# Kernel optimization log

Hardware: AMD Instinct MI355X
Metric: run time of the kernel (lower is better)

## Reference

```python
import jax, jax.numpy as jnp
import numpy as np

RMIN, RMAX = -5.0, 5.0
MIN_BIN, MIN_SLOPE = 1e-4, 1e-4
BATCH, DIM, NBINS, HID = 65536, 64, 8, 128
NLAYERS = 6
SPLIT = DIM // 2  # 32
PDIM = 3 * NBINS + 1  # 25


def _mlp(h, w1, c1, w2, c2, w3, c3, w4, c4):
    # equinox MLP, depth=3: relu on hidden layers, identity on output
    h = jax.nn.relu(h @ w1.T + c1)
    h = jax.nn.relu(h @ w2.T + c2)
    h = jax.nn.relu(h @ w3.T + c3)
    return h @ w4.T + c4


def _rqs_forward(x, params):
    # x: [B,T], params: [B,T,3K+1] -> (y, logdet) each [B,T]
    K = (params.shape[-1] - 1) // 3
    total = RMAX - RMIN
    widths = jax.nn.softmax(params[..., :K], axis=-1) * (total - K * MIN_BIN) + MIN_BIN
    heights = jax.nn.softmax(params[..., K:2 * K], axis=-1) * (total - K * MIN_BIN) + MIN_BIN
    slope_off = float(np.log(np.exp(1.0 - MIN_SLOPE) - 1.0))
    slopes = jax.nn.softplus(params[..., 2 * K:] + slope_off) + MIN_SLOPE  # [B,T,K+1]
    zero = jnp.zeros(widths.shape[:-1] + (1,), widths.dtype)
    x_pos = jnp.concatenate([zero, jnp.cumsum(widths, -1)], -1) + RMIN   # [B,T,K+1]
    y_pos = jnp.concatenate([zero, jnp.cumsum(heights, -1)], -1) + RMIN
    below, above = x < RMIN, x > RMAX
    sl, sr = slopes[..., 0], slopes[..., -1]
    y_lin_l = (x - RMIN) * sl + RMIN
    y_lin_r = (x - RMAX) * sr + RMAX
    # searchsorted(x_pos[1:-1], x, side='right') == count of knots <= x
    bin_idx = jnp.clip(jnp.sum(x_pos[..., 1:-1] <= x[..., None], axis=-1), 0, K - 1)
    take = lambda a, i: jnp.take_along_axis(a, i[..., None], axis=-1)[..., 0]
    x_k, x_k1 = take(x_pos, bin_idx), take(x_pos, bin_idx + 1)
    y_k, y_k1 = take(y_pos, bin_idx), take(y_pos, bin_idx + 1)
    d_k, d_k1 = take(slopes, bin_idx), take(slopes, bin_idx + 1)
    w, h = x_k1 - x_k, y_k1 - y_k
    xi = jnp.clip((x - x_k) / w, 0.0, 1.0)
    s = h / w
    xi1m = 1.0 - xi
    q = xi * xi1m
    num = s * xi * xi + d_k * q
    den = s + (d_k1 + d_k - 2.0 * s) * q
    y_sp = y_k + h * num / den
    deriv = s * s * (d_k1 * xi * xi + 2.0 * s * q + d_k * xi1m * xi1m) / (den * den)
    y = jnp.where(below, y_lin_l, jnp.where(above, y_lin_r, y_sp))
    ld = jnp.where(below, jnp.log(sl), jnp.where(above, jnp.log(sr), jnp.log(deriv)))
    return y, ld


def _coupling(x, w1, c1, w2, c2, w3, c3, w4, c4, midx, tidx):
    xm = x[:, midx]           # [B,32]
    xt = x[:, tidx]           # [B,32]
    params = _mlp(xm, w1, c1, w2, c2, w3, c3, w4, c4)  # [B, 32*25]
    params = params.reshape(xt.shape[0], xt.shape[1], PDIM)
    yt, ld = _rqs_forward(xt, params)
    y = jnp.zeros_like(x).at[:, midx].set(xm).at[:, tidx].set(yt)
    return y, jnp.sum(ld, axis=-1)


def _make_masks():
    half_m = np.arange(0, SPLIT, dtype=np.int32)          # mask==1 positions
    half_t = np.arange(SPLIT, DIM, dtype=np.int32)
    alt_m = np.arange(1, DIM, 2, dtype=np.int32)          # odd -> mask==1
    alt_t = np.arange(0, DIM, 2, dtype=np.int32)
    mi = np.stack([half_m if i % 2 == 0 else alt_m for i in range(NLAYERS)])
    ti = np.stack([half_t if i % 2 == 0 else alt_t for i in range(NLAYERS)])
    return jnp.asarray(mi), jnp.asarray(ti)


def setup_inputs() -> dict:
    key = jax.random.key(0)
    ks = jax.random.split(key, 10)
    sc = 0.05
    x = jax.random.normal(ks[0], (BATCH, DIM), jnp.float32)
    W1 = jax.random.normal(ks[1], (NLAYERS, HID, SPLIT), jnp.float32) * sc
    b1 = jax.random.normal(ks[2], (NLAYERS, HID), jnp.float32) * sc
    W2 = jax.random.normal(ks[3], (NLAYERS, HID, HID), jnp.float32) * sc
    b2 = jax.random.normal(ks[4], (NLAYERS, HID), jnp.float32) * sc
    W3 = jax.random.normal(ks[5], (NLAYERS, HID, HID), jnp.float32) * sc
    b3 = jax.random.normal(ks[6], (NLAYERS, HID), jnp.float32) * sc
    W4 = jax.random.normal(ks[7], (NLAYERS, SPLIT * PDIM, HID), jnp.float32) * sc
    b4 = jax.random.normal(ks[8], (NLAYERS, SPLIT * PDIM), jnp.float32) * sc
    mask_idx, transform_idx = _make_masks()
    return dict(x=x, W1=W1, b1=b1, W2=W2, b2=b2, W3=W3, b3=b3, W4=W4, b4=b4,
                mask_idx=mask_idx, transform_idx=transform_idx)


def reference(x, W1, b1, W2, b2, W3, b3, W4, b4, mask_idx, transform_idx):
    def step(carry, layer):
        xc, tot = carry
        w1, c1, w2, c2, w3, c3, w4, c4, mi, ti = layer
        y, ld = _coupling(xc, w1, c1, w2, c2, w3, c3, w4, c4, mi, ti)
        return (y, tot + ld), None
    init = (x, jnp.zeros(x.shape[0], x.dtype))
    (y, total_logdet), _ = jax.lax.scan(
        step, init, (W1, b1, W2, b2, W3, b3, W4, b4, mask_idx, transform_idx))
    return y, total_logdet
```

## Files before the change

### kernel.cpp

```cpp
#include <hip/hip_runtime.h>
#include <math.h>

#define BATCH   65536
#define DIM     64
#define HID     128
#define SPLIT   32
#define NBINS   8
#define PDIM    25
#define NLAYERS 6
#define R_MIN   (-5.0f)
#define R_MAX   (5.0f)
#define MIN_BIN   1.0e-4f
#define MIN_SLOPE 1.0e-4f
#define SOFF      0.54116666f

#define ROWSW 16
#define WAVES 4
#define MBLK  64
#define NT    256

#define N_W1  (HID*SPLIT)
#define N_W2  (HID*HID)
#define N_W4P (32*32*HID)
#define N_W4  (SPLIT*PDIM*HID)

typedef __attribute__((ext_vector_type(8))) short bf16x8;
typedef __attribute__((ext_vector_type(4))) float f32x4;

__device__ __forceinline__ short f2bf(float f) {
    unsigned u = __builtin_bit_cast(unsigned, f);
    unsigned r = u + 0x7FFFu + ((u >> 16) & 1u);
    return (short)(r >> 16);
}

__device__ __forceinline__ unsigned pk2(float a, float b) {
    unsigned r;
    asm("v_cvt_pk_bf16_f32 %0, %1, %2" : "=v"(r) : "v"(a), "v"(b));
    return r;
}

__device__ __forceinline__ bf16x8 ldfrag(const short* base) {
    short4 lo = *reinterpret_cast<const short4*>(base);
    short4 hi = *reinterpret_cast<const short4*>(base + 64);
    bf16x8 a;
    a[0]=lo.x; a[1]=lo.y; a[2]=lo.z; a[3]=lo.w;
    a[4]=hi.x; a[5]=hi.y; a[6]=hi.z; a[7]=hi.w;
    return a;
}

__global__ void cvt_weights(const float* __restrict__ W1, const float* __restrict__ W2,
                            const float* __restrict__ W3, const float* __restrict__ W4,
                            const float* __restrict__ b4,
                            short* __restrict__ o1, short* __restrict__ o2,
                            short* __restrict__ o3, short* __restrict__ o4,
                            float* __restrict__ b4q) {
    const int stride = gridDim.x * blockDim.x;
    const int i0 = blockIdx.x * blockDim.x + threadIdx.x;
    for (int i = i0; i < NLAYERS*N_W1; i += stride) {
        const int L = i >> 12, rem = i & 4095;
        const int nt = rem >> 9, q = rem & 511;
        const int l = q >> 3, e = q & 7;
        o1[i] = f2bf(W1[L*N_W1 + (nt*16 + (l&15))*SPLIT + (l>>4)*8 + e]);
    }
    for (int i = i0; i < NLAYERS*N_W2; i += stride) {
        const int L = i >> 14, rem = i & 16383;
        const int c = rem >> 9, q = rem & 511;
        const int nt = c >> 2, kt = c & 3;
        const int l = q >> 3, e = q & 7;
        const int src = L*N_W2 + (nt*16 + (l&15))*HID + kt*32 + (l>>4)*8 + e;
        o2[i] = f2bf(W2[src]);
        o3[i] = f2bf(W3[src]);
    }
    for (int i = i0; i < NLAYERS*N_W4P; i += stride) {
        const int L = i >> 17, rem = i & (N_W4P - 1);
        const int c = rem >> 9, q = rem & 511;
        const int tb = c >> 5, pq = (c >> 2) & 7, kt = c & 3;
        const int l = q >> 3, e = q & 7;
        const int t = tb*4 + ((l & 15) >> 2);
        const int p = pq*4 + (l & 3);
        o4[i] = (p < PDIM)
              ? f2bf(W4[(size_t)L*N_W4 + (size_t)(t*PDIM + p)*HID + kt*32 + (l>>4)*8 + e])
              : (short)0;
    }
    for (int i = i0; i < NLAYERS*SPLIT*32; i += stride) {
        const int L = i >> 10, rem = i & 1023;
        const int t = rem >> 5, p = rem & 31;
        b4q[i] = (p < PDIM) ? b4[L*SPLIT*PDIM + t*PDIM + p] : 0.0f;
    }
}

__global__ __launch_bounds__(NT, 4) void flow_layer(
    const float* xin, float* yout, float* logdet, const int first,
    const short* __restrict__ bW1, const float* __restrict__ b1,
    const short* __restrict__ bW2, const float* __restrict__ b2,
    const short* __restrict__ bW3, const float* __restrict__ b3,
    const short* __restrict__ bW4, const float* __restrict__ b4q,
    const int* __restrict__ mi, const int* __restrict__ ti)
{
    __shared__ short act[WAVES][32 * 64];
    __shared__ float xts[WAVES][ROWSW][33];

    const int tid = threadIdx.x;
    const int wv  = tid >> 6;
    const int l   = tid & 63;
    const int lr  = l & 15;
    const int lg  = l >> 4;
    const int rbase = blockIdx.x * MBLK + wv * ROWSW;

    short* const actw = &act[wv][0];

    {
        const int kcol = l & 31;
        const int mc = mi[kcol], tc = ti[kcol];
        const int r0 = l >> 5;
        #pragma unroll
        for (int it = 0; it < 8; ++it) {
            const int r = r0 + it * 2;
            const float* row = xin + (size_t)(rbase + r) * DIM;
            const float mv = row[mc];
            actw[(kcol >> 2)*64 + r*4 + (kcol & 3)] = f2bf(mv);
            xts[wv][r][kcol] = row[tc];
            if (first) yout[(size_t)(rbase + r) * DIM + mc] = mv;
        }
    }

    {
        const bf16x8 afr = ldfrag(&actw[(2*lg)*64 + lr*4]);
        f32x4 c[8];
        #pragma unroll
        for (int nt = 0; nt < 8; ++nt) {
            const float4 bv = *reinterpret_cast<const float4*>(b1 + nt*16 + lg*4);
            c[nt] = (f32x4){bv.x, bv.y, bv.z, bv.w};
        }
        #pragma unroll
        for (int nt = 0; nt < 8; ++nt) {
            const bf16x8 wfr = *reinterpret_cast<const bf16x8*>(bW1 + (size_t)nt*512 + l*8);
            c[nt] = __builtin_amdgcn_mfma_f32_16x16x32_bf16(wfr, afr, c[nt], 0, 0, 0);
        }
        #pragma unroll
        for (int nt = 0; nt < 8; ++nt) {
            const unsigned u0 = pk2(fmaxf(c[nt][0], 0.0f), fmaxf(c[nt][1], 0.0f));
            const unsigned u1 = pk2(fmaxf(c[nt][2], 0.0f), fmaxf(c[nt][3], 0.0f));
            *reinterpret_cast<uint2*>(&actw[(nt*4 + lg)*64 + lr*4]) = (uint2){u0, u1};
        }
    }

    #pragma unroll 1
    for (int ph = 0; ph < 2; ++ph) {
        const short* Wp = ph ? bW3 : bW2;
        const float* bp = ph ? b3  : b2;
        bf16x8 afr[4];
        #pragma unroll
        for (int kt = 0; kt < 4; ++kt)
            afr[kt] = ldfrag(&actw[(kt*8 + 2*lg)*64 + lr*4]);
        f32x4 c[8];
        #pragma unroll
        for (int nt = 0; nt < 8; ++nt) {
            const float4 bv = *reinterpret_cast<const float4*>(bp + nt*16 + lg*4);
            c[nt] = (f32x4){bv.x, bv.y, bv.z, bv.w};
        }
        #pragma unroll
        for (int kt = 0; kt < 4; ++kt)
            #pragma unroll
            for (int nt = 0; nt < 8; ++nt) {
                const bf16x8 wfr = *reinterpret_cast<const bf16x8*>(Wp + (size_t)(nt*4 + kt)*512 + l*8);
                c[nt] = __builtin_amdgcn_mfma_f32_16x16x32_bf16(wfr, afr[kt], c[nt], 0, 0, 0);
            }
        #pragma unroll
        for (int nt = 0; nt < 8; ++nt) {
            const unsigned u0 = pk2(fmaxf(c[nt][0], 0.0f), fmaxf(c[nt][1], 0.0f));
            const unsigned u1 = pk2(fmaxf(c[nt][2], 0.0f), fmaxf(c[nt][3], 0.0f));
            *reinterpret_cast<uint2*>(&actw[(nt*4 + lg)*64 + lr*4]) = (uint2){u0, u1};
        }
    }

    bf16x8 afr[4];
    #pragma unroll
    for (int kt = 0; kt < 4; ++kt)
        afr[kt] = ldfrag(&actw[(kt*8 + 2*lg)*64 + lr*4]);

    float ldacc = 0.0f;
    #pragma unroll 1
    for (int tb = 0; tb < 8; ++tb) {
        const int t = tb*4 + lg;
        f32x4 c[8];
        #pragma unroll
        for (int pq = 0; pq < 8; ++pq) {
            const float4 bv = *reinterpret_cast<const float4*>(b4q + t*32 + pq*4);
            c[pq] = (f32x4){bv.x, bv.y, bv.z, bv.w};
        }
        #pragma unroll
        for (int kt = 0; kt < 4; ++kt)
            #pragma unroll
            for (int pq = 0; pq < 8; ++pq) {
                const bf16x8 wfr = *reinterpret_cast<const bf16x8*>(
                    bW4 + (size_t)((tb*8 + pq)*4 + kt)*512 + l*8);
                c[pq] = __builtin_amdgcn_mfma_f32_16x16x32_bf16(wfr, afr[kt], c[pq], 0, 0, 0);
            }

        float p[32];
        #pragma unroll
        for (int pq = 0; pq < 8; ++pq)
            #pragma unroll
            for (int j = 0; j < 4; ++j) p[pq*4 + j] = c[pq][j];

        float sl[NBINS + 1];
        #pragma unroll
        for (int i = 0; i < NBINS + 1; ++i) {
            const float z = p[2*NBINS + i] + SOFF;
            const float sp = (z > 15.0f) ? z : __logf(1.0f + __expf(z));
            sl[i] = sp + MIN_SLOPE;
        }
        float wd[NBINS];
        {
            float mx = p[0];
            #pragma unroll
            for (int i = 1; i < NBINS; ++i) mx = fmaxf(mx, p[i]);
            float sum = 0.0f;
            #pragma unroll
            for (int i = 0; i < NBINS; ++i) { wd[i] = __expf(p[i] - mx); sum += wd[i]; }
            const float sc = __fdividef((R_MAX - R_MIN) - NBINS * MIN_BIN, sum);
            #pragma unroll
            for (int i = 0; i < NBINS; ++i) wd[i] = wd[i] * sc + MIN_BIN;
        }
        float hg[NBINS];
        {
            float mx = p[NBINS];
            #pragma unroll
            for (int i = 1; i < NBINS; ++i) mx = fmaxf(mx, p[NBINS + i]);
            float sum = 0.0f;
            #pragma unroll
            for (int i = 0; i < NBINS; ++i) { hg[i] = __expf(p[NBINS + i] - mx); sum += hg[i]; }
            const float sc = __fdividef((R_MAX - R_MIN) - NBINS * MIN_BIN, sum);
            #pragma unroll
            for (int i = 0; i < NBINS; ++i) hg[i] = hg[i] * sc + MIN_BIN;
        }

        const float x = xts[wv][lr][t];

        int b = 0;
        {
            float cx = R_MIN;
            #pragma unroll
            for (int i = 1; i < NBINS; ++i) { cx += wd[i-1]; b += (cx <= x) ? 1 : 0; }
        }
        float x_k = R_MIN, y_k = R_MIN, wsel = wd[0], hsel = hg[0], d_k = sl[0], d_k1 = sl[1];
        {
            float cx = R_MIN, cy = R_MIN;
            #pragma unroll
            for (int i = 0; i < NBINS; ++i) {
                if (i == b) { x_k = cx; y_k = cy; wsel = wd[i]; hsel = hg[i];
                              d_k = sl[i]; d_k1 = sl[i+1]; }
                cx += wd[i]; cy += hg[i];
            }
        }

        const float invw = __fdividef(1.0f, wsel);
        float xi = (x - x_k) * invw;
        xi = fminf(fmaxf(xi, 0.0f), 1.0f);
        const float s    = hsel * invw;
        const float xi1m = 1.0f - xi;
        const float q    = xi * xi1m;
        const float num  = s * xi * xi + d_k * q;
        const float den  = s + (d_k1 + d_k - 2.0f * s) * q;
        const float invden = __fdividef(1.0f, den);
        const float y_sp = y_k + hsel * num * invden;
        const float deriv = s * s * (d_k1 * xi * xi + 2.0f * s * q + d_k * xi1m * xi1m)
                            * invden * invden;

        const bool below = x < R_MIN;
        const bool above = x > R_MAX;
        const float yv = below ? ((x - R_MIN) * sl[0]     + R_MIN)
                       : (above ? ((x - R_MAX) * sl[NBINS] + R_MAX) : y_sp);
        const float dv = below ? sl[0] : (above ? sl[NBINS] : deriv);
        ldacc += __logf(dv);

        yout[(size_t)(rbase + lr) * DIM + ti[t]] = yv;
    }

    ldacc += __shfl_xor(ldacc, 16, 64);
    ldacc += __shfl_xor(ldacc, 32, 64);
    if (l < 16) {
        const int row = rbase + lr;
        if (first) logdet[row] = ldacc;
        else       logdet[row] += ldacc;
    }
}

extern "C" void kernel_launch(void* const* d_in, const int* in_sizes, int n_in,
                              void* d_out, int out_size, void* d_ws, size_t ws_size,
                              hipStream_t stream) {
    const float* x  = (const float*)d_in[0];
    const float* W1 = (const float*)d_in[1];
    const float* b1 = (const float*)d_in[2];
    const float* W2 = (const float*)d_in[3];
    const float* b2 = (const float*)d_in[4];
    const float* W3 = (const float*)d_in[5];
    const float* b3 = (const float*)d_in[6];
    const float* W4 = (const float*)d_in[7];
    const float* b4 = (const float*)d_in[8];
    const int*   mi = (const int*)d_in[9];
    const int*   ti = (const int*)d_in[10];

    float* y      = (float*)d_out;
    float* logdet = y + (size_t)BATCH * DIM;

    short* bW1 = (short*)d_ws;
    short* bW2 = bW1 + NLAYERS * N_W1;
    short* bW3 = bW2 + NLAYERS * N_W2;
    short* bW4 = bW3 + NLAYERS * N_W2;
    float* b4q = (float*)(bW4 + (size_t)NLAYERS * N_W4P);

    cvt_weights<<<512, 256, 0, stream>>>(W1, W2, W3, W4, b4, bW1, bW2, bW3, bW4, b4q);

    dim3 grid(BATCH / MBLK), block(NT);
    for (int L = 0; L < NLAYERS; ++L) {
        flow_layer<<<grid, block, 0, stream>>>(
            (L == 0) ? x : y, y, logdet, (L == 0) ? 1 : 0,
            bW1 + (size_t)L * N_W1, b1 + L * HID,
            bW2 + (size_t)L * N_W2, b2 + L * HID,
            bW3 + (size_t)L * N_W2, b3 + L * HID,
            bW4 + (size_t)L * N_W4P, b4q + (size_t)L * SPLIT * 32,
            mi + L * SPLIT, ti + L * SPLIT);
    }
}
```

Baseline: 362.6 us.

## Stage MLP weights in LDS via async DMA with double-buffered W4 prefetch

Weights for all four MLP layers are copied into a shared LDS buffer with global_load_lds, so each block fetches them once instead of every wave reading them from global memory. The W4 tiles are double-buffered: the next output tile is prefetched while the current one is computed, and the matching transform-column x values are prefetched into registers. The all-zero padded parameter quad is no longer computed, cutting output MFMAs from 8 to 7 per tile. In exchange the kernel uses about 80KB of LDS, lowers launch bounds to 2 blocks per CU, and adds block-wide barriers each tile.

```diff
diff --git a/kernel.cpp b/kernel.cpp
--- a/kernel.cpp
+++ b/kernel.cpp
@@ -18,6 +18,7 @@
 #define WAVES 4
 #define MBLK  64
 #define NT    256
+#define W4CH  28
 
 #define N_W1  (HID*SPLIT)
 #define N_W2  (HID*HID)
@@ -37,6 +38,12 @@
     unsigned r;
     asm("v_cvt_pk_bf16_f32 %0, %1, %2" : "=v"(r) : "v"(a), "v"(b));
     return r;
+}
+
+__device__ __forceinline__ void gload16(const short* g, short* s) {
+    __builtin_amdgcn_global_load_lds(
+        (const __attribute__((address_space(1))) void*)g,
+        (__attribute__((address_space(3))) void*)s, 16, 0, 0);
 }
 
 __device__ __forceinline__ bf16x8 ldfrag(const short* base) {
@@ -89,7 +96,7 @@
     }
 }
 
-__global__ __launch_bounds__(NT, 4) void flow_layer(
+__global__ __launch_bounds__(NT, 2) void flow_layer(
     const float* xin, float* yout, float* logdet, const int first,
     const short* __restrict__ bW1, const float* __restrict__ b1,
     const short* __restrict__ bW2, const float* __restrict__ b2,
@@ -97,8 +104,8 @@
     const short* __restrict__ bW4, const float* __restrict__ b4q,
     const int* __restrict__ mi, const int* __restrict__ ti)
 {
+    __shared__ short wbuf[2][16384];
     __shared__ short act[WAVES][32 * 64];
-    __shared__ float xts[WAVES][ROWSW][33];
 
     const int tid = threadIdx.x;
     const int wv  = tid >> 6;
@@ -109,20 +116,30 @@
 
     short* const actw = &act[wv][0];
 
+    #pragma unroll
+    for (int i = 0; i < 2; ++i) {
+        const int c = wv * 2 + i;
+        gload16(bW1 + c * 512 + l * 8, &wbuf[0][c * 512]);
+    }
+    #pragma unroll
+    for (int i = 0; i < 8; ++i) {
+        const int c = wv * 8 + i;
+        gload16(bW2 + c * 512 + l * 8, &wbuf[1][c * 512]);
+    }
+
     {
         const int kcol = l & 31;
-        const int mc = mi[kcol], tc = ti[kcol];
+        const int mc = mi[kcol];
         const int r0 = l >> 5;
         #pragma unroll
         for (int it = 0; it < 8; ++it) {
             const int r = r0 + it * 2;
-            const float* row = xin + (size_t)(rbase + r) * DIM;
-            const float mv = row[mc];
+            const float mv = xin[(size_t)(rbase + r) * DIM + mc];
             actw[(kcol >> 2)*64 + r*4 + (kcol & 3)] = f2bf(mv);
-            xts[wv][r][kcol] = row[tc];
             if (first) yout[(size_t)(rbase + r) * DIM + mc] = mv;
         }
     }
+    __syncthreads();
 
     {
         const bf16x8 afr = ldfrag(&actw[(2*lg)*64 + lr*4]);
@@ -134,7 +151,7 @@
         }
         #pragma unroll
         for (int nt = 0; nt < 8; ++nt) {
-            const bf16x8 wfr = *reinterpret_cast<const bf16x8*>(bW1 + (size_t)nt*512 + l*8);
+            const bf16x8 wfr = *reinterpret_cast<const bf16x8*>(&wbuf[0][nt*512 + l*8]);
             c[nt] = __builtin_amdgcn_mfma_f32_16x16x32_bf16(wfr, afr, c[nt], 0, 0, 0);
         }
         #pragma unroll
@@ -144,11 +161,15 @@
             *reinterpret_cast<uint2*>(&actw[(nt*4 + lg)*64 + lr*4]) = (uint2){u0, u1};
         }
     }
-
-    #pragma unroll 1
-    for (int ph = 0; ph < 2; ++ph) {
-        const short* Wp = ph ? bW3 : bW2;
-        const float* bp = ph ? b3  : b2;
+    __syncthreads();
+
+    #pragma unroll
+    for (int i = 0; i < 8; ++i) {
+        const int c = wv * 8 + i;
+        gload16(bW3 + c * 512 + l * 8, &wbuf[0][c * 512]);
+    }
+
+    {
         bf16x8 afr[4];
         #pragma unroll
         for (int kt = 0; kt < 4; ++kt)
@@ -156,14 +177,47 @@
         f32x4 c[8];
         #pragma unroll
         for (int nt = 0; nt < 8; ++nt) {
-            const float4 bv = *reinterpret_cast<const float4*>(bp + nt*16 + lg*4);
+            const float4 bv = *reinterpret_cast<const float4*>(b2 + nt*16 + lg*4);
             c[nt] = (f32x4){bv.x, bv.y, bv.z, bv.w};
         }
         #pragma unroll
         for (int kt = 0; kt < 4; ++kt)
             #pragma unroll
             for (int nt = 0; nt < 8; ++nt) {
-                const bf16x8 wfr = *reinterpret_cast<const bf16x8*>(Wp + (size_t)(nt*4 + kt)*512 + l*8);
+                const bf16x8 wfr = *reinterpret_cast<const bf16x8*>(&wbuf[1][(nt*4 + kt)*512 + l*8]);
+                c[nt] = __builtin_amdgcn_mfma_f32_16x16x32_bf16(wfr, afr[kt], c[nt], 0, 0, 0);
+            }
+        #pragma unroll
+        for (int nt = 0; nt < 8; ++nt) {
+            const unsigned u0 = pk2(fmaxf(c[nt][0], 0.0f), fmaxf(c[nt][1], 0.0f));
+            const unsigned u1 = pk2(fmaxf(c[nt][2], 0.0f), fmaxf(c[nt][3], 0.0f));
+            *reinterpret_cast<uint2*>(&actw[(nt*4 + lg)*64 + lr*4]) = (uint2){u0, u1};
+        }
+    }
+    __syncthreads();
+
+    #pragma unroll
+    for (int i = 0; i < 7; ++i) {
+        const int c = wv * 7 + i;
+        gload16(bW4 + (size_t)c * 512 + l * 8, &wbuf[1][c * 512]);
+    }
+
+    {
+        bf16x8 afr[4];
+        #pragma unroll
+        for (int kt = 0; kt < 4; ++kt)
+            afr[kt] = ldfrag(&actw[(kt*8 + 2*lg)*64 + lr*4]);
+        f32x4 c[8];
+        #pragma unroll
+        for (int nt = 0; nt < 8; ++nt) {
+            const float4 bv = *reinterpret_cast<const float4*>(b3 + nt*16 + lg*4);
+            c[nt] = (f32x4){bv.x, bv.y, bv.z, bv.w};
+        }
+        #pragma unroll
+        for (int kt = 0; kt < 4; ++kt)
+            #pragma unroll
+            for (int nt = 0; nt < 8; ++nt) {
+                const bf16x8 wfr = *reinterpret_cast<const bf16x8*>(&wbuf[0][(nt*4 + kt)*512 + l*8]);
                 c[nt] = __builtin_amdgcn_mfma_f32_16x16x32_bf16(wfr, afr[kt], c[nt], 0, 0, 0);
             }
         #pragma unroll
@@ -179,28 +233,47 @@
     for (int kt = 0; kt < 4; ++kt)
         afr[kt] = ldfrag(&actw[(kt*8 + 2*lg)*64 + lr*4]);
 
+    __syncthreads();
+
+    const float* rowx = xin + (size_t)(rbase + lr) * DIM;
+    int   tcur = ti[lg];
+    float xcur = rowx[tcur];
+
     float ldacc = 0.0f;
     #pragma unroll 1
     for (int tb = 0; tb < 8; ++tb) {
+        if (tb < 7) {
+            short* wbn = &wbuf[tb & 1][0];
+            #pragma unroll
+            for (int i = 0; i < 7; ++i) {
+                const int c = wv * 7 + i;
+                gload16(bW4 + (size_t)((tb + 1) * 32 + c) * 512 + l * 8, wbn + c * 512);
+            }
+        }
+        int   tnxt = tcur;
+        float xnxt = xcur;
+        if (tb < 7) { tnxt = ti[(tb + 1) * 4 + lg]; xnxt = rowx[tnxt]; }
+
         const int t = tb*4 + lg;
-        f32x4 c[8];
-        #pragma unroll
-        for (int pq = 0; pq < 8; ++pq) {
+        const short* wb = &wbuf[(tb + 1) & 1][0];
+
+        f32x4 c[7];
+        #pragma unroll
+        for (int pq = 0; pq < 7; ++pq) {
             const float4 bv = *reinterpret_cast<const float4*>(b4q + t*32 + pq*4);
             c[pq] = (f32x4){bv.x, bv.y, bv.z, bv.w};
         }
         #pragma unroll
         for (int kt = 0; kt < 4; ++kt)
             #pragma unroll
-            for (int pq = 0; pq < 8; ++pq) {
-                const bf16x8 wfr = *reinterpret_cast<const bf16x8*>(
-                    bW4 + (size_t)((tb*8 + pq)*4 + kt)*512 + l*8);
+            for (int pq = 0; pq < 7; ++pq) {
+                const bf16x8 wfr = *reinterpret_cast<const bf16x8*>(wb + (pq*4 + kt)*512 + l*8);
                 c[pq] = __builtin_amdgcn_mfma_f32_16x16x32_bf16(wfr, afr[kt], c[pq], 0, 0, 0);
             }
 
-        float p[32];
-        #pragma unroll
-        for (int pq = 0; pq < 8; ++pq)
+        float p[28];
+        #pragma unroll
+        for (int pq = 0; pq < 7; ++pq)
             #pragma unroll
             for (int j = 0; j < 4; ++j) p[pq*4 + j] = c[pq][j];
 
@@ -236,7 +309,7 @@
             for (int i = 0; i < NBINS; ++i) hg[i] = hg[i] * sc + MIN_BIN;
         }
 
-        const float x = xts[wv][lr][t];
+        const float x = xcur;
 
         int b = 0;
         {
@@ -275,7 +348,10 @@
         const float dv = below ? sl[0] : (above ? sl[NBINS] : deriv);
         ldacc += __logf(dv);
 
-        yout[(size_t)(rbase + lr) * DIM + ti[t]] = yv;
+        yout[(size_t)(rbase + lr) * DIM + tcur] = yv;
+
+        __syncthreads();
+        tcur = tnxt; xcur = xnxt;
     }
 
     ldacc += __shfl_xor(ldacc, 16, 64);
```

New measurement: 351.7 us. 3.0% less time.

## Trim padded MFMA tile and compute softplus only for selected spline knots

Applied to the files above, without the earlier changes.

The last-layer GEMM now runs 7 column tiles instead of 8, skipping the tile that holds only padding beyond PDIM. The spline epilogue drops max-subtraction from both softmaxes, fuses the bin search with knot selection using selects, and evaluates softplus only for the two chosen slopes and the two boundary slopes instead of all nine. The per-row loop is templated with an optional unroll-by-2, and a different variant is chosen per layer. The aim is fewer MFMAs and transcendental ops in the epilogue. Removing max-subtraction gives up overflow protection for large logits, and the per-layer variant choice looks tuned to one measurement.

```diff
diff --git a/kernel.cpp b/kernel.cpp
--- a/kernel.cpp
+++ b/kernel.cpp
@@ -89,6 +89,7 @@
     }
 }
 
+template<int UNR>
 __global__ __launch_bounds__(NT, 4) void flow_layer(
     const float* xin, float* yout, float* logdet, const int first,
     const short* __restrict__ bW1, const float* __restrict__ b1,
@@ -180,80 +181,60 @@
         afr[kt] = ldfrag(&actw[(kt*8 + 2*lg)*64 + lr*4]);
 
     float ldacc = 0.0f;
-    #pragma unroll 1
-    for (int tb = 0; tb < 8; ++tb) {
+
+    auto body = [&](const int tb) {
         const int t = tb*4 + lg;
-        f32x4 c[8];
-        #pragma unroll
-        for (int pq = 0; pq < 8; ++pq) {
+        f32x4 c[7];
+        #pragma unroll
+        for (int pq = 0; pq < 7; ++pq) {
             const float4 bv = *reinterpret_cast<const float4*>(b4q + t*32 + pq*4);
             c[pq] = (f32x4){bv.x, bv.y, bv.z, bv.w};
         }
         #pragma unroll
         for (int kt = 0; kt < 4; ++kt)
             #pragma unroll
-            for (int pq = 0; pq < 8; ++pq) {
+            for (int pq = 0; pq < 7; ++pq) {
                 const bf16x8 wfr = *reinterpret_cast<const bf16x8*>(
                     bW4 + (size_t)((tb*8 + pq)*4 + kt)*512 + l*8);
                 c[pq] = __builtin_amdgcn_mfma_f32_16x16x32_bf16(wfr, afr[kt], c[pq], 0, 0, 0);
             }
 
-        float p[32];
-        #pragma unroll
-        for (int pq = 0; pq < 8; ++pq)
-            #pragma unroll
-            for (int j = 0; j < 4; ++j) p[pq*4 + j] = c[pq][j];
-
-        float sl[NBINS + 1];
-        #pragma unroll
-        for (int i = 0; i < NBINS + 1; ++i) {
-            const float z = p[2*NBINS + i] + SOFF;
-            const float sp = (z > 15.0f) ? z : __logf(1.0f + __expf(z));
-            sl[i] = sp + MIN_SLOPE;
-        }
-        float wd[NBINS];
-        {
-            float mx = p[0];
-            #pragma unroll
-            for (int i = 1; i < NBINS; ++i) mx = fmaxf(mx, p[i]);
-            float sum = 0.0f;
-            #pragma unroll
-            for (int i = 0; i < NBINS; ++i) { wd[i] = __expf(p[i] - mx); sum += wd[i]; }
-            const float sc = __fdividef((R_MAX - R_MIN) - NBINS * MIN_BIN, sum);
-            #pragma unroll
-            for (int i = 0; i < NBINS; ++i) wd[i] = wd[i] * sc + MIN_BIN;
-        }
-        float hg[NBINS];
-        {
-            float mx = p[NBINS];
-            #pragma unroll
-            for (int i = 1; i < NBINS; ++i) mx = fmaxf(mx, p[NBINS + i]);
-            float sum = 0.0f;
-            #pragma unroll
-            for (int i = 0; i < NBINS; ++i) { hg[i] = __expf(p[NBINS + i] - mx); sum += hg[i]; }
-            const float sc = __fdividef((R_MAX - R_MIN) - NBINS * MIN_BIN, sum);
-            #pragma unroll
-            for (int i = 0; i < NBINS; ++i) hg[i] = hg[i] * sc + MIN_BIN;
-        }
+#define P(i) c[(i)>>2][(i)&3]
+        float wd[NBINS], hg[NBINS];
+        float sw = 0.0f, sh = 0.0f;
+        #pragma unroll
+        for (int i = 0; i < NBINS; ++i) { wd[i] = __expf(P(i));         sw += wd[i]; }
+        #pragma unroll
+        for (int i = 0; i < NBINS; ++i) { hg[i] = __expf(P(NBINS + i)); sh += hg[i]; }
+        const float scw = __fdividef((R_MAX - R_MIN) - NBINS * MIN_BIN, sw);
+        const float sch = __fdividef((R_MAX - R_MIN) - NBINS * MIN_BIN, sh);
+        #pragma unroll
+        for (int i = 0; i < NBINS; ++i) { wd[i] = wd[i]*scw + MIN_BIN; hg[i] = hg[i]*sch + MIN_BIN; }
 
         const float x = xts[wv][lr][t];
 
-        int b = 0;
-        {
-            float cx = R_MIN;
-            #pragma unroll
-            for (int i = 1; i < NBINS; ++i) { cx += wd[i-1]; b += (cx <= x) ? 1 : 0; }
-        }
-        float x_k = R_MIN, y_k = R_MIN, wsel = wd[0], hsel = hg[0], d_k = sl[0], d_k1 = sl[1];
-        {
-            float cx = R_MIN, cy = R_MIN;
-            #pragma unroll
-            for (int i = 0; i < NBINS; ++i) {
-                if (i == b) { x_k = cx; y_k = cy; wsel = wd[i]; hsel = hg[i];
-                              d_k = sl[i]; d_k1 = sl[i+1]; }
-                cx += wd[i]; cy += hg[i];
-            }
-        }
+        float cx = R_MIN, cy = R_MIN;
+        float x_k = R_MIN, y_k = R_MIN, wsel = wd[0], hsel = hg[0];
+        float z0 = P(16), z1 = P(17);
+        #pragma unroll
+        for (int i = 1; i < NBINS; ++i) {
+            cx += wd[i-1]; cy += hg[i-1];
+            const bool tk = (cx <= x);
+            x_k  = tk ? cx        : x_k;
+            y_k  = tk ? cy        : y_k;
+            wsel = tk ? wd[i]     : wsel;
+            hsel = tk ? hg[i]     : hsel;
+            z0   = tk ? P(16 + i) : z0;
+            z1   = tk ? P(17 + i) : z1;
+        }
+
+        auto sp = [](float v) {
+            const float z = v + SOFF;
+            return ((z > 15.0f) ? z : __logf(1.0f + __expf(z))) + MIN_SLOPE;
+        };
+        const float d_k = sp(z0), d_k1 = sp(z1);
+        const float sl0 = sp(P(16)), sl8 = sp(P(24));
+#undef P
 
         const float invw = __fdividef(1.0f, wsel);
         float xi = (x - x_k) * invw;
@@ -270,12 +251,20 @@
 
         const bool below = x < R_MIN;
         const bool above = x > R_MAX;
-        const float yv = below ? ((x - R_MIN) * sl[0]     + R_MIN)
-                       : (above ? ((x - R_MAX) * sl[NBINS] + R_MAX) : y_sp);
-        const float dv = below ? sl[0] : (above ? sl[NBINS] : deriv);
+        const float yv = below ? ((x - R_MIN) * sl0 + R_MIN)
+                       : (above ? ((x - R_MAX) * sl8 + R_MAX) : y_sp);
+        const float dv = below ? sl0 : (above ? sl8 : deriv);
         ldacc += __logf(dv);
 
         yout[(size_t)(rbase + lr) * DIM + ti[t]] = yv;
+    };
+
+    if constexpr (UNR == 1) {
+        #pragma unroll 1
+        for (int tb = 0; tb < 8; ++tb) body(tb);
+    } else {
+        #pragma unroll 1
+        for (int tb = 0; tb < 8; tb += 2) { body(tb); body(tb + 1); }
     }
 
     ldacc += __shfl_xor(ldacc, 16, 64);
@@ -315,12 +304,20 @@
 
     dim3 grid(BATCH / MBLK), block(NT);
     for (int L = 0; L < NLAYERS; ++L) {
-        flow_layer<<<grid, block, 0, stream>>>(
-            (L == 0) ? x : y, y, logdet, (L == 0) ? 1 : 0,
-            bW1 + (size_t)L * N_W1, b1 + L * HID,
-            bW2 + (size_t)L * N_W2, b2 + L * HID,
-            bW3 + (size_t)L * N_W2, b3 + L * HID,
-            bW4 + (size_t)L * N_W4P, b4q + (size_t)L * SPLIT * 32,
-            mi + L * SPLIT, ti + L * SPLIT);
-    }
-}
+        const float* in = (L == 0) ? x : y;
+        const int first = (L == 0) ? 1 : 0;
+        const short* w1 = bW1 + (size_t)L * N_W1;
+        const short* w2 = bW2 + (size_t)L * N_W2;
+        const short* w3 = bW3 + (size_t)L * N_W2;
+        const short* w4 = bW4 + (size_t)L * N_W4P;
+        const float* bb1 = b1 + L * HID, *bb2 = b2 + L * HID, *bb3 = b3 + L * HID;
+        const float* bq = b4q + (size_t)L * SPLIT * 32;
+        const int* mil = mi + L * SPLIT, *til = ti + L * SPLIT;
+        if (L == 0 || L == 1 || L == 4)
+            flow_layer<1><<<grid, block, 0, stream>>>(in, y, logdet, first,
+                w1, bb1, w2, bb2, w3, bb3, w4, bq, mil, til);
+        else
+            flow_layer<2><<<grid, block, 0, stream>>>(in, y, logdet, first,
+                w1, bb1, w2, bb2, w3, bb3, w4, bq, mil, til);
+    }
+}
```

Result: faster. 349.6 us (-3.6%).
